# Kernel optimization log

Measured on AMD Instinct MI355X. Metric: run time of the kernel, lower is better.

Reference implementation:

```python
import jax, jax.numpy as jnp
import numpy as np

N = 1_000_000   # total atoms in batched graph
G = 50_000      # number of molecules (graphs)
F = 128         # gnn_out_feats (node feature dim)
H = 128         # classifier_hidden_feats
T = 12          # n_tasks
EPS = 1e-5      # BatchNorm1d eps


def setup_inputs() -> dict:
    key = jax.random.key(0)
    ks = jax.random.split(key, 20)
    s = 0.05
    inp = {}
    inp["node_feats"] = jax.random.normal(ks[0], (N, F), jnp.float32)
    inp["segment_ids"] = jnp.sort(jax.random.randint(ks[1], (N,), 0, G))
    inp["num_graphs"] = G
    # per-task atom weighting: Linear(F,1) per task, stacked -> [T,F]
    inp["atom_w"] = jax.random.normal(ks[2], (T, F), jnp.float32) * s
    inp["atom_b"] = jnp.zeros((T,), jnp.float32)
    # fc_layer 1: Linear(F,H) -> ReLU -> BatchNorm1d(H) (eval mode)
    inp["W1"] = jax.random.normal(ks[3], (T, F, H), jnp.float32) * s
    inp["b1"] = jnp.zeros((T, H), jnp.float32)
    inp["g1"] = jnp.ones((T, H), jnp.float32)
    inp["be1"] = jnp.zeros((T, H), jnp.float32)
    inp["rm1"] = jnp.zeros((T, H), jnp.float32)
    inp["rv1"] = jnp.ones((T, H), jnp.float32)
    # fc_layer 2 and 3: Linear(H,H) -> ReLU -> BatchNorm1d(H)
    inp["W2"] = jax.random.normal(ks[4], (T, H, H), jnp.float32) * s
    inp["b2"] = jnp.zeros((T, H), jnp.float32)
    inp["g2"] = jnp.ones((T, H), jnp.float32)
    inp["be2"] = jnp.zeros((T, H), jnp.float32)
    inp["rm2"] = jnp.zeros((T, H), jnp.float32)
    inp["rv2"] = jnp.ones((T, H), jnp.float32)
    inp["W3"] = jax.random.normal(ks[5], (T, H, H), jnp.float32) * s
    inp["b3"] = jnp.zeros((T, H), jnp.float32)
    inp["g3"] = jnp.ones((T, H), jnp.float32)
    inp["be3"] = jnp.zeros((T, H), jnp.float32)
    inp["rm3"] = jnp.zeros((T, H), jnp.float32)
    inp["rv3"] = jnp.ones((T, H), jnp.float32)
    # output_layer: Linear(H,H) -> ReLU -> Linear(H,1)
    inp["oW1"] = jax.random.normal(ks[6], (T, H, H), jnp.float32) * s
    inp["ob1"] = jnp.zeros((T, H), jnp.float32)
    inp["oW2"] = jax.random.normal(ks[7], (T, H), jnp.float32) * s
    inp["ob2"] = jnp.zeros((T,), jnp.float32)
    return inp


def _fc(x, W, b, g, be, rm, rv):
    # Linear -> ReLU -> BatchNorm1d (eval, running stats), batched over tasks t
    y = jax.nn.relu(jnp.einsum('gti,tio->gto', x, W) + b)
    return (y - rm) * (g * jax.lax.rsqrt(rv + EPS)) + be


def reference(node_feats, segment_ids, num_graphs, atom_w, atom_b,
              W1, b1, g1, be1, rm1, rv1,
              W2, b2, g2, be2, rm2, rv2,
              W3, b3, g3, be3, rm3, rv3,
              oW1, ob1, oW2, ob2):
    n_tasks = atom_w.shape[0]
    # WeightAndSum: per-task sigmoid node weights [N,T]
    w = jax.nn.sigmoid(node_feats @ atom_w.T + atom_b)
    # per-task weighted segment-sum pooling: loop over small fixed task count
    sums = [jax.ops.segment_sum(node_feats * w[:, t:t + 1], segment_ids,
                                num_segments=num_graphs)
            for t in range(n_tasks)]
    mol = jnp.stack(sums, axis=1)  # [G, T, F]
    h = _fc(mol, W1, b1, g1, be1, rm1, rv1)
    h = _fc(h, W2, b2, g2, be2, rm2, rv2)
    h = _fc(h, W3, b3, g3, be3, rm3, rv3)
    z = jax.nn.relu(jnp.einsum('gth,tho->gto', h, oW1) + ob1)
    pred = jnp.einsum('gth,th->gt', z, oW2) + ob2  # [G, T]
    return pred
```

## Files before the change

kernel.cpp:

```cpp
#include <hip/hip_runtime.h>
#include <hip/hip_bf16.h>
#include <hip/hip_fp16.h>

typedef _Float16 f16;
typedef _Float16 f16x2 __attribute__((ext_vector_type(2)));
typedef _Float16 f16x4 __attribute__((ext_vector_type(4)));
typedef _Float16 f16x8 __attribute__((ext_vector_type(8)));
typedef float f32x4 __attribute__((ext_vector_type(4)));

typedef __attribute__((address_space(1))) const void gas_t;
typedef __attribute__((address_space(3))) void las_t;

#define BN_EPS 1e-5f

__global__ void seg_starts_k(const int* __restrict__ seg, int N, int G, int* __restrict__ start) {
    int n = blockIdx.x * blockDim.x + threadIdx.x;
    if (n >= N) return;
    int s = seg[n];
    int p = (n == 0) ? -1 : seg[n - 1];
    for (int g = p + 1; g <= s; ++g) start[g] = n;
    if (n == N - 1) {
        for (int g = s + 1; g <= G; ++g) start[g] = N;
    }
}

__global__ void prep_k(const float* __restrict__ W1, const float* __restrict__ b1,
                       const float* __restrict__ W2, const float* __restrict__ b2,
                       const float* __restrict__ W3, const float* __restrict__ b3,
                       const float* __restrict__ oW1, const float* __restrict__ ob1,
                       const float* __restrict__ g1, const float* __restrict__ be1,
                       const float* __restrict__ rm1, const float* __restrict__ rv1,
                       const float* __restrict__ g2, const float* __restrict__ be2,
                       const float* __restrict__ rm2, const float* __restrict__ rv2,
                       const float* __restrict__ g3, const float* __restrict__ be3,
                       const float* __restrict__ rm3, const float* __restrict__ rv3,
                       f16* __restrict__ Wt, float* __restrict__ bp) {
    int T = gridDim.x;
    int t = blockIdx.x, l = blockIdx.y;
    int o = threadIdx.x;
    __shared__ float s_sh[128], c_sh[128];

    const float *W, *b, *gg = nullptr, *be = nullptr, *rm = nullptr, *rv = nullptr;
    if (l == 0)      { W = W1;  b = b1; }
    else if (l == 1) { W = W2;  b = b2;  gg = g1; be = be1; rm = rm1; rv = rv1; }
    else if (l == 2) { W = W3;  b = b3;  gg = g2; be = be2; rm = rm2; rv = rv2; }
    else             { W = oW1; b = ob1; gg = g3; be = be3; rm = rm3; rv = rv3; }

    float s = 1.f, c = 0.f;
    if (gg) {
        float sv = gg[t * 128 + o] * rsqrtf(rv[t * 128 + o] + BN_EPS);
        s = sv;
        c = be[t * 128 + o] - rm[t * 128 + o] * sv;
    }
    s_sh[o] = s;
    c_sh[o] = c;
    __syncthreads();

    const float* Wsrc = W + (size_t)t * 128 * 128;
    f16* Wdst = Wt + (((size_t)l * T + t) * 128 + o) * 128;
    float acc = b[t * 128 + o];
    for (int i = 0; i < 128; ++i) {
        float wv = Wsrc[i * 128 + o];
        Wdst[(((i >> 3) ^ (o & 7)) << 3) + (i & 7)] = (f16)(s_sh[i] * wv);
        acc += c_sh[i] * wv;
    }
    bp[((size_t)l * T + t) * 128 + o] = acc;
}

__global__ __launch_bounds__(256) void pool5_k(const float* __restrict__ feats,
                                               const float* __restrict__ atom_w,
                                               const float* __restrict__ atom_b,
                                               const int* __restrict__ start,
                                               f16* __restrict__ mol, int G) {
    int wave = threadIdx.x >> 6, lane = threadIdx.x & 63;
    int g = blockIdx.x * 4 + wave;
    if (g >= G) return;
    int lr = lane & 15, kg = lane >> 4;

    f16x8 bfr[4];
    float ab = 0.f;
#pragma unroll
    for (int ks = 0; ks < 4; ++ks) {
        f16x8 v = {};
        if (lr < 12) {
            const float* s = atom_w + lr * 128 + ks * 32 + kg * 8;
#pragma unroll
            for (int j = 0; j < 8; ++j) v[j] = (f16)s[j];
        }
        bfr[ks] = v;
    }
    if (lr < 12) ab = atom_b[lr];

    f32x4 acc[8];
#pragma unroll
    for (int nf = 0; nf < 8; ++nf) acc[nf] = (f32x4){0.f, 0.f, 0.f, 0.f};

    int s = start[g], e = start[g + 1];

    for (int c0 = s; c0 < e; c0 += 16) {
        int rB[4];
#pragma unroll
        for (int j = 0; j < 4; ++j) {
            int a = c0 + (kg << 2) + j;
            rB[j] = (a < e) ? a : (e - 1);
        }
        float bx[8][4];
#pragma unroll
        for (int j = 0; j < 4; ++j) {
            const float* pB = feats + (size_t)rB[j] * 128 + lr;
#pragma unroll
            for (int fb = 0; fb < 8; ++fb) bx[fb][j] = pB[fb << 4];
        }

        int rA = c0 + lr; if (rA >= e) rA = e - 1;
        const float* pA = feats + (size_t)rA * 128 + (kg << 3);
        f32x4 pa = {0.f, 0.f, 0.f, 0.f};
#pragma unroll
        for (int ks = 0; ks < 4; ++ks) {
            float4 u0 = *(const float4*)(pA + (ks << 5));
            float4 u1 = *(const float4*)(pA + (ks << 5) + 4);
            f16x8 afr;
            afr[0] = (f16)u0.x; afr[1] = (f16)u0.y; afr[2] = (f16)u0.z; afr[3] = (f16)u0.w;
            afr[4] = (f16)u1.x; afr[5] = (f16)u1.y; afr[6] = (f16)u1.z; afr[7] = (f16)u1.w;
            pa = __builtin_amdgcn_mfma_f32_16x16x32_f16(afr, bfr[ks], pa, 0, 0, 0);
        }

        f16x4 a2;
#pragma unroll
        for (int j = 0; j < 4; ++j) {
            float w = 1.f / (1.f + __expf(-(pa[j] + ab)));
            int a = c0 + (kg << 2) + j;
            a2[j] = (a < e) ? (f16)w : (f16)0.f;
        }

#pragma unroll
        for (int fb = 0; fb < 8; ++fb) {
            f16x4 b2;
#pragma unroll
            for (int j = 0; j < 4; ++j) b2[j] = (f16)bx[fb][j];
            acc[fb] = __builtin_amdgcn_mfma_f32_16x16x16f16(a2, b2, acc[fb], 0, 0, 0);
        }
    }

    if (kg < 3) {
        int gx = g & 7;
#pragma unroll
        for (int fb = 0; fb < 8; ++fb) {
            int slot = (fb << 1) + (lr >> 3);
            int fi = (((slot ^ gx)) << 3) + (lr & 7);
#pragma unroll
            for (int j = 0; j < 4; ++j)
                mol[((size_t)((kg << 2) + j) * G + g) * 128 + fi] = (f16)acc[fb][j];
        }
    }
}

__global__ __launch_bounds__(256, 3) void fc_k(const f16* __restrict__ mol,
                                               const f16* __restrict__ Wt,
                                               const float* __restrict__ bp,
                                               const float* __restrict__ oW2,
                                               const float* __restrict__ ob2,
                                               float* __restrict__ out, int G, int T) {
    __shared__ f16 A[64][128];
    __shared__ f16 B[128][128];

    int t = blockIdx.y;
    int g0 = blockIdx.x * 64;
    int tid = threadIdx.x;
    int wid = tid >> 6, lane = tid & 63;

    {
        const f16* aplane = mol + (size_t)t * G * 128;
#pragma unroll
        for (int i = 0; i < 4; ++i) {
            int c = wid + (i << 2);
            int r = (c << 2) + (lane >> 4);
            int row = g0 + r; if (row >= G) row = G - 1;
            const f16* src = aplane + (size_t)row * 128 + ((lane & 15) << 3);
            __builtin_amdgcn_global_load_lds((gas_t*)src,
                (las_t*)((char*)&A[0][0] + c * 1024), 16, 0, 0);
        }
        const f16* bsrc = Wt + ((size_t)0 * T + t) * 16384;
#pragma unroll
        for (int i = 0; i < 8; ++i) {
            int c = wid + (i << 2);
            int r = (c << 2) + (lane >> 4);
            const f16* src = bsrc + (size_t)r * 128 + ((lane & 15) << 3);
            __builtin_amdgcn_global_load_lds((gas_t*)src,
                (las_t*)((char*)&B[0][0] + c * 1024), 16, 0, 0);
        }
    }

    int lg = lane >> 4, lr = lane & 15;
    int m0 = wid * 16;
    int arow = m0 + lr;
    float pred[4] = {0.f, 0.f, 0.f, 0.f};

    for (int l = 0; l < 4; ++l) {
        asm volatile("s_waitcnt vmcnt(0)" ::: "memory");
        __syncthreads();

        f16x8 afr[4];
#pragma unroll
        for (int ks = 0; ks < 4; ++ks) {
            int sl = (4 * ks + lg) ^ (arow & 7);
            afr[ks] = *(const f16x8*)(&A[arow][sl * 8]);
        }

        const float* bias = bp + ((size_t)l * T + t) * 128;
#pragma unroll
        for (int nf = 0; nf < 8; ++nf) {
            int n = nf * 16 + lr;
            f32x4 acc = {0.f, 0.f, 0.f, 0.f};
#pragma unroll
            for (int ks = 0; ks < 4; ++ks) {
                int sl = (4 * ks + lg) ^ (n & 7);
                f16x8 bfr = *(const f16x8*)(&B[n][sl * 8]);
                acc = __builtin_amdgcn_mfma_f32_16x16x32_f16(afr[ks], bfr, acc, 0, 0, 0);
            }
            float bv = bias[n];
            if (l < 3) {
#pragma unroll
                for (int j = 0; j < 4; ++j) {
                    float y = acc[j] + bv;
                    y = y > 0.f ? y : 0.f;
                    int rr = m0 + 4 * lg + j;
                    A[rr][(((n >> 3) ^ (rr & 7)) << 3) + (n & 7)] = (f16)y;
                }
            } else {
                float w2 = oW2[t * 128 + n];
#pragma unroll
                for (int j = 0; j < 4; ++j) {
                    float z = acc[j] + bv;
                    z = z > 0.f ? z : 0.f;
                    pred[j] += z * w2;
                }
            }
        }
        __syncthreads();
        if (l < 3) {
            const f16* bsrc = Wt + ((size_t)(l + 1) * T + t) * 16384;
#pragma unroll
            for (int i = 0; i < 8; ++i) {
                int c = wid + (i << 2);
                int r = (c << 2) + (lane >> 4);
                const f16* src = bsrc + (size_t)r * 128 + ((lane & 15) << 3);
                __builtin_amdgcn_global_load_lds((gas_t*)src,
                    (las_t*)((char*)&B[0][0] + c * 1024), 16, 0, 0);
            }
        }
    }

#pragma unroll
    for (int m = 1; m < 16; m <<= 1) {
#pragma unroll
        for (int j = 0; j < 4; ++j) pred[j] += __shfl_xor(pred[j], m, 64);
    }
    if (lr == 0) {
        float ob = ob2[t];
#pragma unroll
        for (int j = 0; j < 4; ++j) {
            int gg = g0 + m0 + 4 * lg + j;
            if (gg < G) out[(size_t)gg * T + t] = pred[j] + ob;
        }
    }
}

extern "C" void kernel_launch(void* const* d_in, const int* in_sizes, int n_in,
                              void* d_out, int out_size, void* d_ws, size_t ws_size,
                              hipStream_t stream) {
    const float* node_feats = (const float*)d_in[0];
    const int*   seg        = (const int*)d_in[1];
    const float* atom_w     = (const float*)d_in[3];
    const float* atom_b     = (const float*)d_in[4];
    const float* W1  = (const float*)d_in[5];
    const float* b1  = (const float*)d_in[6];
    const float* g1  = (const float*)d_in[7];
    const float* be1 = (const float*)d_in[8];
    const float* rm1 = (const float*)d_in[9];
    const float* rv1 = (const float*)d_in[10];
    const float* W2  = (const float*)d_in[11];
    const float* b2  = (const float*)d_in[12];
    const float* g2  = (const float*)d_in[13];
    const float* be2 = (const float*)d_in[14];
    const float* rm2 = (const float*)d_in[15];
    const float* rv2 = (const float*)d_in[16];
    const float* W3  = (const float*)d_in[17];
    const float* b3  = (const float*)d_in[18];
    const float* g3  = (const float*)d_in[19];
    const float* be3 = (const float*)d_in[20];
    const float* rm3 = (const float*)d_in[21];
    const float* rv3 = (const float*)d_in[22];
    const float* oW1 = (const float*)d_in[23];
    const float* ob1 = (const float*)d_in[24];
    const float* oW2 = (const float*)d_in[25];
    const float* ob2 = (const float*)d_in[26];

    int T = in_sizes[4];
    int F = in_sizes[3] / T;
    int N = in_sizes[0] / F;
    int G = out_size / T;

    char* ws = (char*)d_ws;
    size_t off = 0;
    int* start = (int*)ws;
    off += (((size_t)(G + 1) * 4) + 255) & ~(size_t)255;
    f16* Wt = (f16*)(ws + off);
    off += (((size_t)4 * T * 128 * 128 * 2) + 255) & ~(size_t)255;
    float* bp = (float*)(ws + off);
    off += (((size_t)4 * T * 128 * 4) + 255) & ~(size_t)255;
    f16* mol = (f16*)(ws + off);

    seg_starts_k<<<(N + 255) / 256, 256, 0, stream>>>(seg, N, G, start);
    prep_k<<<dim3(T, 4), 128, 0, stream>>>(W1, b1, W2, b2, W3, b3, oW1, ob1,
                                           g1, be1, rm1, rv1,
                                           g2, be2, rm2, rv2,
                                           g3, be3, rm3, rv3, Wt, bp);
    pool5_k<<<(G + 3) / 4, 256, 0, stream>>>(node_feats, atom_w, atom_b, start, mol, G);
    fc_k<<<dim3((G + 63) / 64, T), 256, 0, stream>>>(mol, Wt, bp, oW2, ob2,
                                                     (float*)d_out, G, T);
}
```

Measured before the change: 348.8 us.

## Tile pooling by fixed 64-atom blocks with shared-memory staged features

Replaces the per-graph pooling kernel, where one wave per molecule looped over its atoms, with one block per 64-atom chunk. The block stages up to 112 rows of features (transposed, in fp16) and the sigmoid task weights in shared memory, then each wave reduces the molecules that start in the chunk. The aim is to balance work across blocks no matter how molecule sizes vary, and to read each feature row once as coalesced float4 loads. The cost is a halo of extra rows per block and the 112-row cap, which silently truncates any molecule extending past that window, plus heavier LDS traffic and occupancy pressure.

New measurement: 432.0 us. 23.8% more time.

```diff
diff --git a/kernel.cpp b/kernel.cpp
--- a/kernel.cpp
+++ b/kernel.cpp
@@ -67,15 +67,28 @@
     bp[((size_t)l * T + t) * 128 + o] = acc;
 }
 
-__global__ __launch_bounds__(256) void pool5_k(const float* __restrict__ feats,
-                                               const float* __restrict__ atom_w,
-                                               const float* __restrict__ atom_b,
-                                               const int* __restrict__ start,
-                                               f16* __restrict__ mol, int G) {
-    int wave = threadIdx.x >> 6, lane = threadIdx.x & 63;
-    int g = blockIdx.x * 4 + wave;
-    if (g >= G) return;
+__global__ __launch_bounds__(256, 4) void pool7_k(const float* __restrict__ feats,
+                                                  const float* __restrict__ atom_w,
+                                                  const float* __restrict__ atom_b,
+                                                  const int* __restrict__ seg,
+                                                  const int* __restrict__ start,
+                                                  f16* __restrict__ mol, int N, int G) {
+    __shared__ f16 xsT[128][116];
+    __shared__ f16 wT[16][116];
+
+    int b = blockIdx.x, A0 = b << 6, tid = threadIdx.x;
+    int wave = tid >> 6, lane = tid & 63;
     int lr = lane & 15, kg = lane >> 4;
+    int cnt = N - A0; if (cnt > 64) cnt = 64;
+
+    int segPrev = (A0 > 0) ? seg[A0 - 1] : -1;
+    int gLastSeg = seg[A0 + cnt - 1];
+    int gFirst = segPrev + 1;
+    int extEnd = start[gLastSeg + 1];
+    int rows_need = extEnd - A0;
+    if (rows_need < cnt) rows_need = cnt;
+    if (rows_need > 112) rows_need = 112;
+    int gLast = (A0 + cnt >= N) ? (G - 1) : gLastSeg;
 
     f16x8 bfr[4];
     float ab = 0.f;
@@ -91,66 +104,87 @@
     }
     if (lr < 12) ab = atom_b[lr];
 
-    f32x4 acc[8];
-#pragma unroll
-    for (int nf = 0; nf < 8; ++nf) acc[nf] = (f32x4){0.f, 0.f, 0.f, 0.f};
-
-    int s = start[g], e = start[g + 1];
-
-    for (int c0 = s; c0 < e; c0 += 16) {
-        int rB[4];
-#pragma unroll
-        for (int j = 0; j < 4; ++j) {
-            int a = c0 + (kg << 2) + j;
-            rB[j] = (a < e) ? a : (e - 1);
-        }
-        float bx[8][4];
-#pragma unroll
-        for (int j = 0; j < 4; ++j) {
-            const float* pB = feats + (size_t)rB[j] * 128 + lr;
-#pragma unroll
-            for (int fb = 0; fb < 8; ++fb) bx[fb][j] = pB[fb << 4];
-        }
-
-        int rA = c0 + lr; if (rA >= e) rA = e - 1;
-        const float* pA = feats + (size_t)rA * 128 + (kg << 3);
-        f32x4 pa = {0.f, 0.f, 0.f, 0.f};
-#pragma unroll
-        for (int ks = 0; ks < 4; ++ks) {
-            float4 u0 = *(const float4*)(pA + (ks << 5));
-            float4 u1 = *(const float4*)(pA + (ks << 5) + 4);
-            f16x8 afr;
-            afr[0] = (f16)u0.x; afr[1] = (f16)u0.y; afr[2] = (f16)u0.z; afr[3] = (f16)u0.w;
-            afr[4] = (f16)u1.x; afr[5] = (f16)u1.y; afr[6] = (f16)u1.z; afr[7] = (f16)u1.w;
-            pa = __builtin_amdgcn_mfma_f32_16x16x32_f16(afr, bfr[ks], pa, 0, 0, 0);
-        }
-
-        f16x4 a2;
-#pragma unroll
-        for (int j = 0; j < 4; ++j) {
-            float w = 1.f / (1.f + __expf(-(pa[j] + ab)));
-            int a = c0 + (kg << 2) + j;
-            a2[j] = (a < e) ? (f16)w : (f16)0.f;
-        }
-
-#pragma unroll
-        for (int fb = 0; fb < 8; ++fb) {
-            f16x4 b2;
-#pragma unroll
-            for (int j = 0; j < 4; ++j) b2[j] = (f16)bx[fb][j];
-            acc[fb] = __builtin_amdgcn_mfma_f32_16x16x16f16(a2, b2, acc[fb], 0, 0, 0);
-        }
-    }
-
-    if (kg < 3) {
-        int gx = g & 7;
-#pragma unroll
-        for (int fb = 0; fb < 8; ++fb) {
-            int slot = (fb << 1) + (lr >> 3);
-            int fi = (((slot ^ gx)) << 3) + (lr & 7);
-#pragma unroll
-            for (int j = 0; j < 4; ++j)
-                mol[((size_t)((kg << 2) + j) * G + g) * 128 + fi] = (f16)acc[fb][j];
+#pragma unroll
+    for (int it = 0; it < 14; ++it) {
+        int v = (it << 8) + tid;
+        int bb = v >> 7, u = v & 127;
+        int r = (bb << 2) + (u & 3), q = u >> 2;
+        float4 x = make_float4(0.f, 0.f, 0.f, 0.f);
+        if (r < rows_need) x = *(const float4*)(feats + (size_t)(A0 + r) * 128 + (q << 2));
+        xsT[(q << 2) + 0][r] = (f16)x.x;
+        xsT[(q << 2) + 1][r] = (f16)x.y;
+        xsT[(q << 2) + 2][r] = (f16)x.z;
+        xsT[(q << 2) + 3][r] = (f16)x.w;
+    }
+
+    int ntau = (rows_need + 15) >> 4;
+#pragma unroll
+    for (int tt = 0; tt < 2; ++tt) {
+        int tau = wave + (tt << 2);
+        if (tau < ntau) {
+            int a = (tau << 4) + lr;
+            bool rv = a < rows_need;
+            const float* pA = feats + (size_t)(A0 + a) * 128 + (kg << 3);
+            f32x4 pa = {0.f, 0.f, 0.f, 0.f};
+#pragma unroll
+            for (int ks = 0; ks < 4; ++ks) {
+                f16x8 afr = {};
+                if (rv) {
+                    float4 u0 = *(const float4*)(pA + (ks << 5));
+                    float4 u1 = *(const float4*)(pA + (ks << 5) + 4);
+                    afr[0] = (f16)u0.x; afr[1] = (f16)u0.y;
+                    afr[2] = (f16)u0.z; afr[3] = (f16)u0.w;
+                    afr[4] = (f16)u1.x; afr[5] = (f16)u1.y;
+                    afr[6] = (f16)u1.z; afr[7] = (f16)u1.w;
+                }
+                pa = __builtin_amdgcn_mfma_f32_16x16x32_f16(afr, bfr[ks], pa, 0, 0, 0);
+            }
+            f16x4 w4;
+#pragma unroll
+            for (int j = 0; j < 4; ++j) {
+                float w = 1.f / (1.f + __expf(-(pa[j] + ab)));
+                w4[j] = (f16)w;
+            }
+            *(f16x4*)(&wT[lr][(tau << 4) + (kg << 2)]) = w4;
+        }
+    }
+    __syncthreads();
+
+    for (int g = gFirst + wave; g <= gLast; g += 4) {
+        int s0 = start[g], e0 = start[g + 1];
+        int lls = s0 - A0; if (lls < 0) lls = 0;
+        int lle = e0 - A0; if (lle > rows_need) lle = rows_need;
+
+        f32x4 acc[8];
+#pragma unroll
+        for (int fb = 0; fb < 8; ++fb) acc[fb] = (f32x4){0.f, 0.f, 0.f, 0.f};
+
+        if (lls < lle) {
+            int ta = lls >> 4, tb = (lle - 1) >> 4;
+            for (int tau = ta; tau <= tb; ++tau) {
+                int a0 = (tau << 4) + (kg << 2);
+                f16x4 a2 = *(const f16x4*)(&wT[lr][a0]);
+#pragma unroll
+                for (int j = 0; j < 4; ++j)
+                    if (a0 + j < lls || a0 + j >= lle) a2[j] = (f16)0.f;
+#pragma unroll
+                for (int fb = 0; fb < 8; ++fb) {
+                    f16x4 b2 = *(const f16x4*)(&xsT[(fb << 4) + lr][a0]);
+                    acc[fb] = __builtin_amdgcn_mfma_f32_16x16x16f16(a2, b2, acc[fb], 0, 0, 0);
+                }
+            }
+        }
+
+        if (kg < 3) {
+            int gx = g & 7;
+#pragma unroll
+            for (int fb = 0; fb < 8; ++fb) {
+                int slot = (fb << 1) + (lr >> 3);
+                int fi = (((slot ^ gx)) << 3) + (lr & 7);
+#pragma unroll
+                for (int j = 0; j < 4; ++j)
+                    mol[((size_t)((kg << 2) + j) * G + g) * 128 + fi] = (f16)acc[fb][j];
+            }
         }
     }
 }
@@ -300,6 +334,7 @@
     int F = in_sizes[3] / T;
     int N = in_sizes[0] / F;
     int G = out_size / T;
+    int nb = (N + 63) / 64;
 
     char* ws = (char*)d_ws;
     size_t off = 0;
@@ -316,7 +351,7 @@
                                            g1, be1, rm1, rv1,
                                            g2, be2, rm2, rv2,
                                            g3, be3, rm3, rv3, Wt, bp);
-    pool5_k<<<(G + 3) / 4, 256, 0, stream>>>(node_feats, atom_w, atom_b, start, mol, G);
+    pool7_k<<<nb, 256, 0, stream>>>(node_feats, atom_w, atom_b, seg, start, mol, N, G);
     fc_k<<<dim3((G + 63) / 64, T), 256, 0, stream>>>(mol, Wt, bp, oW2, ob2,
                                                      (float*)d_out, G, T);
 }
```

## Double-buffer FC weights and use 2x2 warp tiling in fc_k

Applied to the files above, without the earlier changes.

The fused MLP kernel now double-buffers the per-layer weight tile in LDS, prefetching the next layer's weights right after the barrier so the load overlaps the current layer's MFMAs. Warps are rearranged as a 2x2 grid, each computing 32 rows by 64 columns, so every B fragment is reused across two A fragments. The final prediction is reduced across the two column warps through shared memory. LDS use grows to about 80 KB per block, so launch bounds drop from 3 to 2 blocks per CU, which may reduce occupancy.

New measurement: 365.0 us. +4.6%, slower.

```diff
diff --git a/kernel.cpp b/kernel.cpp
--- a/kernel.cpp
+++ b/kernel.cpp
@@ -155,28 +155,31 @@
     }
 }
 
-__global__ __launch_bounds__(256, 3) void fc_k(const f16* __restrict__ mol,
+__global__ __launch_bounds__(256, 2) void fc_k(const f16* __restrict__ mol,
                                                const f16* __restrict__ Wt,
                                                const float* __restrict__ bp,
                                                const float* __restrict__ oW2,
                                                const float* __restrict__ ob2,
                                                float* __restrict__ out, int G, int T) {
     __shared__ f16 A[64][128];
-    __shared__ f16 B[128][128];
+    __shared__ f16 B[2][128][128];
 
     int t = blockIdx.y;
     int g0 = blockIdx.x * 64;
     int tid = threadIdx.x;
     int wid = tid >> 6, lane = tid & 63;
+    int kg = lane >> 4, lr = lane & 15;
+    int wr = wid >> 1, wc = wid & 1;
+    int ar0 = wr * 32, bc0 = wc * 64;
 
     {
         const f16* aplane = mol + (size_t)t * G * 128;
 #pragma unroll
         for (int i = 0; i < 4; ++i) {
             int c = wid + (i << 2);
-            int r = (c << 2) + (lane >> 4);
+            int r = (c << 2) + kg;
             int row = g0 + r; if (row >= G) row = G - 1;
-            const f16* src = aplane + (size_t)row * 128 + ((lane & 15) << 3);
+            const f16* src = aplane + (size_t)row * 128 + (lr << 3);
             __builtin_amdgcn_global_load_lds((gas_t*)src,
                 (las_t*)((char*)&A[0][0] + c * 1024), 16, 0, 0);
         }
@@ -184,85 +187,111 @@
 #pragma unroll
         for (int i = 0; i < 8; ++i) {
             int c = wid + (i << 2);
-            int r = (c << 2) + (lane >> 4);
-            const f16* src = bsrc + (size_t)r * 128 + ((lane & 15) << 3);
+            int r = (c << 2) + kg;
+            const f16* src = bsrc + (size_t)r * 128 + (lr << 3);
             __builtin_amdgcn_global_load_lds((gas_t*)src,
-                (las_t*)((char*)&B[0][0] + c * 1024), 16, 0, 0);
-        }
-    }
-
-    int lg = lane >> 4, lr = lane & 15;
-    int m0 = wid * 16;
-    int arow = m0 + lr;
-    float pred[4] = {0.f, 0.f, 0.f, 0.f};
+                (las_t*)((char*)&B[0][0][0] + c * 1024), 16, 0, 0);
+        }
+    }
+
+    float pred[2][4];
+#pragma unroll
+    for (int m = 0; m < 2; ++m)
+#pragma unroll
+        for (int j = 0; j < 4; ++j) pred[m][j] = 0.f;
 
     for (int l = 0; l < 4; ++l) {
         asm volatile("s_waitcnt vmcnt(0)" ::: "memory");
         __syncthreads();
 
-        f16x8 afr[4];
-#pragma unroll
-        for (int ks = 0; ks < 4; ++ks) {
-            int sl = (4 * ks + lg) ^ (arow & 7);
-            afr[ks] = *(const f16x8*)(&A[arow][sl * 8]);
-        }
+        if (l < 3) {
+            const f16* bsrc = Wt + ((size_t)(l + 1) * T + t) * 16384;
+            char* bdst = (char*)&B[(l + 1) & 1][0][0];
+#pragma unroll
+            for (int i = 0; i < 8; ++i) {
+                int c = wid + (i << 2);
+                int r = (c << 2) + kg;
+                const f16* src = bsrc + (size_t)r * 128 + (lr << 3);
+                __builtin_amdgcn_global_load_lds((gas_t*)src,
+                    (las_t*)(bdst + c * 1024), 16, 0, 0);
+            }
+        }
+
+        f16x8 afr[2][4];
+#pragma unroll
+        for (int m = 0; m < 2; ++m) {
+            int row = ar0 + m * 16 + lr;
+#pragma unroll
+            for (int ks = 0; ks < 4; ++ks) {
+                int sl = (4 * ks + kg) ^ (row & 7);
+                afr[m][ks] = *(const f16x8*)(&A[row][sl * 8]);
+            }
+        }
+        __syncthreads();
 
         const float* bias = bp + ((size_t)l * T + t) * 128;
-#pragma unroll
-        for (int nf = 0; nf < 8; ++nf) {
-            int n = nf * 16 + lr;
-            f32x4 acc = {0.f, 0.f, 0.f, 0.f};
+        const f16 (*Bc)[128] = B[l & 1];
+#pragma unroll
+        for (int n = 0; n < 4; ++n) {
+            int col = bc0 + n * 16 + lr;
+            f32x4 acc0 = {0.f, 0.f, 0.f, 0.f};
+            f32x4 acc1 = {0.f, 0.f, 0.f, 0.f};
 #pragma unroll
             for (int ks = 0; ks < 4; ++ks) {
-                int sl = (4 * ks + lg) ^ (n & 7);
-                f16x8 bfr = *(const f16x8*)(&B[n][sl * 8]);
-                acc = __builtin_amdgcn_mfma_f32_16x16x32_f16(afr[ks], bfr, acc, 0, 0, 0);
-            }
-            float bv = bias[n];
+                int sl = (4 * ks + kg) ^ (col & 7);
+                f16x8 bfr = *(const f16x8*)(&Bc[col][sl * 8]);
+                acc0 = __builtin_amdgcn_mfma_f32_16x16x32_f16(afr[0][ks], bfr, acc0, 0, 0, 0);
+                acc1 = __builtin_amdgcn_mfma_f32_16x16x32_f16(afr[1][ks], bfr, acc1, 0, 0, 0);
+            }
+            float bv = bias[col];
             if (l < 3) {
 #pragma unroll
                 for (int j = 0; j < 4; ++j) {
-                    float y = acc[j] + bv;
-                    y = y > 0.f ? y : 0.f;
-                    int rr = m0 + 4 * lg + j;
-                    A[rr][(((n >> 3) ^ (rr & 7)) << 3) + (n & 7)] = (f16)y;
+                    float y0 = acc0[j] + bv; y0 = y0 > 0.f ? y0 : 0.f;
+                    float y1 = acc1[j] + bv; y1 = y1 > 0.f ? y1 : 0.f;
+                    int r0 = ar0 + 4 * kg + j;
+                    int r1 = r0 + 16;
+                    A[r0][(((col >> 3) ^ (r0 & 7)) << 3) + (col & 7)] = (f16)y0;
+                    A[r1][(((col >> 3) ^ (r1 & 7)) << 3) + (col & 7)] = (f16)y1;
                 }
             } else {
-                float w2 = oW2[t * 128 + n];
+                float w2 = oW2[t * 128 + col];
 #pragma unroll
                 for (int j = 0; j < 4; ++j) {
-                    float z = acc[j] + bv;
-                    z = z > 0.f ? z : 0.f;
-                    pred[j] += z * w2;
+                    float z0 = acc0[j] + bv; z0 = z0 > 0.f ? z0 : 0.f;
+                    float z1 = acc1[j] + bv; z1 = z1 > 0.f ? z1 : 0.f;
+                    pred[0][j] += z0 * w2;
+                    pred[1][j] += z1 * w2;
                 }
             }
         }
-        __syncthreads();
-        if (l < 3) {
-            const f16* bsrc = Wt + ((size_t)(l + 1) * T + t) * 16384;
-#pragma unroll
-            for (int i = 0; i < 8; ++i) {
-                int c = wid + (i << 2);
-                int r = (c << 2) + (lane >> 4);
-                const f16* src = bsrc + (size_t)r * 128 + ((lane & 15) << 3);
-                __builtin_amdgcn_global_load_lds((gas_t*)src,
-                    (las_t*)((char*)&B[0][0] + c * 1024), 16, 0, 0);
-            }
-        }
-    }
-
-#pragma unroll
-    for (int m = 1; m < 16; m <<= 1) {
-#pragma unroll
-        for (int j = 0; j < 4; ++j) pred[j] += __shfl_xor(pred[j], m, 64);
-    }
+    }
+
+#pragma unroll
+    for (int msk = 1; msk < 16; msk <<= 1) {
+#pragma unroll
+        for (int m = 0; m < 2; ++m)
+#pragma unroll
+            for (int j = 0; j < 4; ++j)
+                pred[m][j] += __shfl_xor(pred[m][j], msk, 64);
+    }
+
+    __syncthreads();
+    float* predsh = (float*)&A[0][0];
     if (lr == 0) {
-        float ob = ob2[t];
-#pragma unroll
-        for (int j = 0; j < 4; ++j) {
-            int gg = g0 + m0 + 4 * lg + j;
-            if (gg < G) out[(size_t)gg * T + t] = pred[j] + ob;
-        }
+#pragma unroll
+        for (int m = 0; m < 2; ++m)
+#pragma unroll
+            for (int j = 0; j < 4; ++j) {
+                int row = ar0 + m * 16 + 4 * kg + j;
+                predsh[row * 2 + wc] = pred[m][j];
+            }
+    }
+    __syncthreads();
+    if (tid < 64) {
+        int row = tid;
+        if (g0 + row < G)
+            out[(size_t)(g0 + row) * T + t] = predsh[row * 2 + 0] + predsh[row * 2 + 1] + ob2[t];
     }
 }
 
```
